# Kernel optimization log

Hardware: AMD Instinct MI355X
Metric: run time of the kernel (lower is better)

Reference implementation:

```python
import jax, jax.numpy as jnp
import numpy as np

KH, KW = 4, 4
N, P, IN_CH, OUT_CH = 50000, 32, 64, 64


def setup_inputs() -> dict:
    key = jax.random.key(0)
    k1, k2, k3, k4 = jax.random.split(key, 4)
    features = jax.random.normal(k1, (N, IN_CH), jnp.float32)
    receivers = jax.random.randint(k2, (N, P), 0, N)
    # relative offsets scaled so most neighbors fall inside the support radius
    relative_positions = jax.random.normal(k3, (N, P, 2), jnp.float32) * 0.35
    window_support = jnp.float32(1.0)
    a = 3  # window exponent (1 - d^2/R^2)^a
    kernel = jax.random.uniform(k4, (KH, KW, IN_CH, OUT_CH), jnp.float32, -0.05, 0.05)
    bias = jnp.zeros((OUT_CH,), jnp.float32)
    return {"features": features, "receivers": receivers,
            "relative_positions": relative_positions,
            "window_support": window_support, "a": a,
            "kernel": kernel, "bias": bias}


def reference(features, receivers, relative_positions, window_support, a, kernel, bias):
    kh, kw, in_ch, out_ch = kernel.shape
    n, p = receivers.shape
    g_bins = kh * kw

    gathered = features[receivers]                      # [N,P,in] gather
    r = relative_positions / window_support             # normalized to [-1,1]
    d2 = jnp.sum(r * r, axis=-1)                        # [N,P]
    win = jnp.maximum(1.0 - d2, 0.0) ** a               # radial window

    # map normalized position to continuous kernel-grid coordinates
    gy = jnp.clip((r[..., 0] + 1.0) * 0.5 * (kh - 1), 0.0, kh - 1)
    gx = jnp.clip((r[..., 1] + 1.0) * 0.5 * (kw - 1), 0.0, kw - 1)
    y0 = jnp.clip(jnp.floor(gy).astype(jnp.int32), 0, kh - 2)
    x0 = jnp.clip(jnp.floor(gx).astype(jnp.int32), 0, kw - 2)
    fy = gy - y0
    fx = gx - x0

    # accumulate window*bilinear-weighted features into kernel bins per output point,
    # avoiding materializing a per-edge [in,out] interpolated filter
    n_idx = jnp.arange(n)[:, None]                      # broadcasts over P
    M = jnp.zeros((n, g_bins, in_ch), features.dtype)
    corners = [(0, 0, (1 - fy) * (1 - fx)), (0, 1, (1 - fy) * fx),
               (1, 0, fy * (1 - fx)), (1, 1, fy * fx)]
    for dy, dx, bw in corners:
        g = (y0 + dy) * kw + (x0 + dx)                  # [N,P] flat bin index
        M = M.at[n_idx, g].add((bw * win)[..., None] * gathered)

    out = jnp.einsum('ngi,gio->no', M, kernel.reshape(g_bins, in_ch, out_ch))
    return out / p + bias
```

## Files before the change

kernel.cpp:

```cpp
#include <hip/hip_runtime.h>
#include <hip/hip_bf16.h>

typedef unsigned short u16;
typedef unsigned int u32;

#define THREADS 512
constexpr int CH = 64;
constexpr int PP = 32;
constexpr int TM = 16;

constexpr int W_OFF  = 0;
constexpr int RB_OFF = 0;
constexpr int MB_OFF = 16384;
constexpr int LDS_BYTES = 49152;

typedef __attribute__((ext_vector_type(8))) short short8;
typedef __attribute__((ext_vector_type(4))) float f32x4;

static __device__ __forceinline__ u16 f2bf_rne(float f) {
  __hip_bfloat16 h = __float2bfloat16(f);
  return __builtin_bit_cast(u16, h);
}
static __device__ __forceinline__ u16 rbf(float f) {
  u32 u = __builtin_bit_cast(u32, f);
  return (u16)((u + 0x8000u) >> 16);
}

__global__ void prep_all(const float* __restrict__ feat, u16* __restrict__ fbf,
                         const float* __restrict__ kern, u16* __restrict__ k2f,
                         int nq) {
  int i = blockIdx.x * blockDim.x + threadIdx.x;
  if (i < nq) {
    const int row = i >> 4, l15 = i & 15;
    const float* src = feat + (size_t)row * 64 + l15;
    const u32 a0 = f2bf_rne(src[0]);
    const u32 a1 = f2bf_rne(src[16]);
    const u32 a2 = f2bf_rne(src[32]);
    const u32 a3 = f2bf_rne(src[48]);
    uint2 w; w.x = a0 | (a1 << 16); w.y = a2 | (a3 << 16);
    ((uint2*)fbf)[i] = w;
  } else {
    const int d = i - nq;
    if (d < 65536) {
      const int e = d & 7, l = (d >> 3) & 63, ot = (d >> 9) & 3, ks = d >> 11;
      const int k = ks * 32 + (l >> 4) * 8 + e;
      const int o = ot * 16 + (l & 15);
      k2f[d] = f2bf_rne(kern[k * 64 + o]);
    }
  }
}

__global__ __launch_bounds__(THREADS, 6) void cconv_main(
    const int* __restrict__ recv, const float* __restrict__ relpos,
    const float* __restrict__ wsup, const int* __restrict__ aptr,
    const u16* __restrict__ fbf, const u16* __restrict__ k2f,
    const float* __restrict__ bias, float* __restrict__ out) {
  __shared__ __align__(16) char smem[LDS_BYTES];
  const int tid = threadIdx.x;
  const int n0 = blockIdx.x * TM;
  const int wid = tid >> 6, lane = tid & 63;
  const int l15 = lane & 15, l4 = lane >> 4;
  const int pairp = wid & 3;
  const int half  = wid >> 2;
  const char* fb2 = (const char*)fbf;

  const int* rp0 = recv + (n0 + wid * 2) * PP + l4 * 8;
  const int4 A40 = *(const int4*)rp0;
  const int4 B40 = *(const int4*)(rp0 + 4);
  const int4 A41 = *(const int4*)(rp0 + PP);
  const int4 B41 = *(const int4*)(rp0 + PP + 4);
  const int rv0[8] = {A40.x, A40.y, A40.z, A40.w, B40.x, B40.y, B40.z, B40.w};
  const int rv1[8] = {A41.x, A41.y, A41.z, A41.w, B41.x, B41.y, B41.z, B41.w};
  uint2 q20[8], q21[8];
  #pragma unroll
  for (int e = 0; e < 8; ++e)
    q20[e] = *(const uint2*)(fb2 + (size_t)(u32)rv0[e] * 128u + (u32)l15 * 8u);
  #pragma unroll
  for (int e = 0; e < 8; ++e)
    q21[e] = *(const uint2*)(fb2 + (size_t)(u32)rv1[e] * 128u + (u32)l15 * 8u);

  {
    const float invws = 1.0f / wsup[0];
    int a = aptr[0];
    if (a < 0 || a > 64) a = (int)(*(const float*)aptr);
    const int e = tid;
    const int m = e >> 5, p = e & 31;
    const int ei = (n0 + m) * PP + p;
    const float2 rp2 = ((const float2*)relpos)[ei];
    const float rx = rp2.x * invws, ry = rp2.y * invws;
    const float d2 = rx * rx + ry * ry;
    const float w1 = fmaxf(1.0f - d2, 0.0f);
    float win = 1.0f;
    for (int q = 0; q < a; ++q) win *= w1;
    float gy = fminf(fmaxf((rx + 1.0f) * 1.5f, 0.0f), 3.0f);
    float gx = fminf(fmaxf((ry + 1.0f) * 1.5f, 0.0f), 3.0f);
    int y0 = (int)gy; y0 = y0 > 2 ? 2 : y0;
    int x0 = (int)gx; x0 = x0 > 2 ? 2 : x0;
    const float fy = gy - (float)y0, fx = gx - (float)x0;
    u16* wp = (u16*)(smem + W_OFF) + m * 512 + p;
    #pragma unroll
    for (int g = 0; g < 16; ++g) {
      const int y = g >> 2, x = g & 3;
      const float wyv = (y == y0) ? (1.0f - fy) : (y == y0 + 1) ? fy : 0.0f;
      const float wxv = (x == x0) ? (1.0f - fx) : (x == x0 + 1) ? fx : 0.0f;
      wp[g * 32] = rbf(win * wyv * wxv);
    }
  }

  #pragma unroll
  for (int t = 0; t < 2; ++t) {
    const int m = wid * 2 + t;
    const short8 af = *(const short8*)(smem + W_OFF + m * 1024 + l15 * 64 + l4 * 16);
    const uint2* q2 = (t == 0) ? q20 : q21;
    f32x4 accm[4];
    const f32x4 cz = {0.f, 0.f, 0.f, 0.f};
    union { u32 u[4]; short8 s; } bb;
    #pragma unroll
    for (int j = 0; j < 4; ++j)
      bb.u[j] = (q2[2 * j].x & 0xffffu) | (q2[2 * j + 1].x << 16);
    accm[0] = __builtin_amdgcn_mfma_f32_16x16x32_bf16(af, bb.s, cz, 0, 0, 0);
    #pragma unroll
    for (int j = 0; j < 4; ++j)
      bb.u[j] = (q2[2 * j].x >> 16) | (q2[2 * j + 1].x & 0xffff0000u);
    accm[1] = __builtin_amdgcn_mfma_f32_16x16x32_bf16(af, bb.s, cz, 0, 0, 0);
    #pragma unroll
    for (int j = 0; j < 4; ++j)
      bb.u[j] = (q2[2 * j].y & 0xffffu) | (q2[2 * j + 1].y << 16);
    accm[2] = __builtin_amdgcn_mfma_f32_16x16x32_bf16(af, bb.s, cz, 0, 0, 0);
    #pragma unroll
    for (int j = 0; j < 4; ++j)
      bb.u[j] = (q2[2 * j].y >> 16) | (q2[2 * j + 1].y & 0xffff0000u);
    accm[3] = __builtin_amdgcn_mfma_f32_16x16x32_bf16(af, bb.s, cz, 0, 0, 0);
    #pragma unroll
    for (int ib = 0; ib < 4; ++ib)
      #pragma unroll
      for (int r = 0; r < 4; ++r) {
        const int g = l4 * 4 + r;
        const u32 k = (u32)(g * 64 + ib * 16 + l15);
        u32 byt = (u32)m * 2048u + k * 2u;
        byt ^= ((u32)((m & 7) ^ (g & 7)) << 4);
        *(u16*)(smem + MB_OFF + byt) = rbf(accm[ib][r]);
      }
  }
  __syncthreads();

  f32x4 acc = {0.f, 0.f, 0.f, 0.f};
  {
    const u32 rowb = (u32)l15 * 2048u;
    const u32 swl = (u32)(l15 & 7) << 4;
    #pragma unroll 8
    for (int j = 0; j < 16; ++j) {
      const int ks = half * 16 + j;
      const u32 kc = (u32)ks * 32u + (u32)l4 * 8u;
      const u32 g7 = (((kc >> 6) & 7u) << 4);
      const u32 byt = (rowb + kc * 2u) ^ swl ^ g7;
      const short8 a2 = *(const short8*)(smem + MB_OFF + byt);
      const short8 b2 = *(const short8*)(k2f + ((u32)(ks * 4 + pairp) * 64u + (u32)lane) * 8u);
      acc = __builtin_amdgcn_mfma_f32_16x16x32_bf16(a2, b2, acc, 0, 0, 0);
    }
  }

  if (half == 1) {
    #pragma unroll
    for (int r = 0; r < 4; ++r) {
      const int row = l4 * 4 + r;
      const u32 byt = (u32)pairp * 1024u + (u32)row * 64u + (u32)((l15 ^ l4) * 4);
      *(float*)(smem + RB_OFF + byt) = acc[r];
    }
  }
  __syncthreads();
  if (half == 0) {
    #pragma unroll
    for (int r = 0; r < 4; ++r) {
      const int row = l4 * 4 + r;
      const u32 byt = (u32)pairp * 1024u + (u32)row * 64u + (u32)((l15 ^ l4) * 4);
      acc[r] += *(const float*)(smem + RB_OFF + byt);
    }
    const int o = pairp * 16 + l15;
    const float bv = bias[o];
    #pragma unroll
    for (int r = 0; r < 4; ++r)
      out[(n0 + l4 * 4 + r) * CH + o] = acc[r] * (1.0f / 32.0f) + bv;
  }
}

extern "C" void kernel_launch(void* const* d_in, const int* in_sizes, int n_in,
                              void* d_out, int out_size, void* d_ws, size_t ws_size,
                              hipStream_t stream) {
  const float* features = (const float*)d_in[0];
  const int* receivers  = (const int*)d_in[1];
  const float* relpos   = (const float*)d_in[2];
  const float* wsup     = (const float*)d_in[3];
  const int* aptr       = (const int*)d_in[4];
  const float* kern     = (const float*)d_in[5];
  const float* bias     = (const float*)d_in[6];
  float* out = (float*)d_out;

  const int N = in_sizes[0] / CH;
  u16* fbf = (u16*)d_ws;
  u16* k2f = (u16*)((char*)d_ws + (size_t)N * CH * 2);

  const int nq = N * 16;
  const int prep_total = nq + 65536;
  prep_all<<<dim3((prep_total + 255) / 256), dim3(256), 0, stream>>>(
      features, fbf, kern, k2f, nq);

  cconv_main<<<dim3(N / TM), dim3(THREADS), 0, stream>>>(
      receivers, relpos, wsup, aptr, fbf, k2f, bias, out);
}
```

Measured before the change: 48.76 us.

## Make main kernel persistent and keep filter weights resident in registers

The main kernel now runs on a fixed grid of 625 blocks. Each block loops over several 16-point tiles instead of handling a single one. The bf16 filter fragments, bias, window scale and exponent are loaded once per block, with the filter kept in 16 short8 registers, instead of being re-read from global memory for every tile. The reduction buffer moves to its own LDS region so it does not clash with the next tile's window writes, and the launch bound drops from 6 to 4 blocks per CU. The goal is less repeated filter traffic and less per-block setup, at the cost of higher register pressure, fewer resident waves to hide the gather latency, and no overlap between tiles within a block.

```diff
diff --git a/kernel.cpp b/kernel.cpp
--- a/kernel.cpp
+++ b/kernel.cpp
@@ -8,11 +8,12 @@
 constexpr int CH = 64;
 constexpr int PP = 32;
 constexpr int TM = 16;
+constexpr int GRID = 625;
 
 constexpr int W_OFF  = 0;
-constexpr int RB_OFF = 0;
 constexpr int MB_OFF = 16384;
-constexpr int LDS_BYTES = 49152;
+constexpr int RB_OFF = 49152;
+constexpr int LDS_BYTES = 53248;
 
 typedef __attribute__((ext_vector_type(8))) short short8;
 typedef __attribute__((ext_vector_type(4))) float f32x4;
@@ -50,137 +51,147 @@
   }
 }
 
-__global__ __launch_bounds__(THREADS, 6) void cconv_main(
+__global__ __launch_bounds__(THREADS, 4) void cconv_main(
     const int* __restrict__ recv, const float* __restrict__ relpos,
     const float* __restrict__ wsup, const int* __restrict__ aptr,
     const u16* __restrict__ fbf, const u16* __restrict__ k2f,
-    const float* __restrict__ bias, float* __restrict__ out) {
+    const float* __restrict__ bias, float* __restrict__ out, int ntile) {
   __shared__ __align__(16) char smem[LDS_BYTES];
   const int tid = threadIdx.x;
-  const int n0 = blockIdx.x * TM;
   const int wid = tid >> 6, lane = tid & 63;
   const int l15 = lane & 15, l4 = lane >> 4;
   const int pairp = wid & 3;
   const int half  = wid >> 2;
   const char* fb2 = (const char*)fbf;
 
-  const int* rp0 = recv + (n0 + wid * 2) * PP + l4 * 8;
-  const int4 A40 = *(const int4*)rp0;
-  const int4 B40 = *(const int4*)(rp0 + 4);
-  const int4 A41 = *(const int4*)(rp0 + PP);
-  const int4 B41 = *(const int4*)(rp0 + PP + 4);
-  const int rv0[8] = {A40.x, A40.y, A40.z, A40.w, B40.x, B40.y, B40.z, B40.w};
-  const int rv1[8] = {A41.x, A41.y, A41.z, A41.w, B41.x, B41.y, B41.z, B41.w};
-  uint2 q20[8], q21[8];
+  short8 b2r[16];
   #pragma unroll
-  for (int e = 0; e < 8; ++e)
-    q20[e] = *(const uint2*)(fb2 + (size_t)(u32)rv0[e] * 128u + (u32)l15 * 8u);
-  #pragma unroll
-  for (int e = 0; e < 8; ++e)
-    q21[e] = *(const uint2*)(fb2 + (size_t)(u32)rv1[e] * 128u + (u32)l15 * 8u);
-
-  {
-    const float invws = 1.0f / wsup[0];
-    int a = aptr[0];
-    if (a < 0 || a > 64) a = (int)(*(const float*)aptr);
-    const int e = tid;
-    const int m = e >> 5, p = e & 31;
-    const int ei = (n0 + m) * PP + p;
-    const float2 rp2 = ((const float2*)relpos)[ei];
-    const float rx = rp2.x * invws, ry = rp2.y * invws;
-    const float d2 = rx * rx + ry * ry;
-    const float w1 = fmaxf(1.0f - d2, 0.0f);
-    float win = 1.0f;
-    for (int q = 0; q < a; ++q) win *= w1;
-    float gy = fminf(fmaxf((rx + 1.0f) * 1.5f, 0.0f), 3.0f);
-    float gx = fminf(fmaxf((ry + 1.0f) * 1.5f, 0.0f), 3.0f);
-    int y0 = (int)gy; y0 = y0 > 2 ? 2 : y0;
-    int x0 = (int)gx; x0 = x0 > 2 ? 2 : x0;
-    const float fy = gy - (float)y0, fx = gx - (float)x0;
-    u16* wp = (u16*)(smem + W_OFF) + m * 512 + p;
+  for (int j = 0; j < 16; ++j)
+    b2r[j] = *(const short8*)(k2f +
+        ((u32)((half * 16 + j) * 4 + pairp) * 64u + (u32)lane) * 8u);
+
+  const float invws = 1.0f / wsup[0];
+  int aexp = aptr[0];
+  if (aexp < 0 || aexp > 64) aexp = (int)(*(const float*)aptr);
+  const float bv = bias[pairp * 16 + l15];
+
+  for (int tile = blockIdx.x; tile < ntile; tile += GRID) {
+    const int n0 = tile * TM;
+
+    const int* rp0 = recv + (n0 + wid * 2) * PP + l4 * 8;
+    const int4 A40 = *(const int4*)rp0;
+    const int4 B40 = *(const int4*)(rp0 + 4);
+    const int4 A41 = *(const int4*)(rp0 + PP);
+    const int4 B41 = *(const int4*)(rp0 + PP + 4);
+    const int rv0[8] = {A40.x, A40.y, A40.z, A40.w, B40.x, B40.y, B40.z, B40.w};
+    const int rv1[8] = {A41.x, A41.y, A41.z, A41.w, B41.x, B41.y, B41.z, B41.w};
+    uint2 q20[8], q21[8];
     #pragma unroll
-    for (int g = 0; g < 16; ++g) {
-      const int y = g >> 2, x = g & 3;
-      const float wyv = (y == y0) ? (1.0f - fy) : (y == y0 + 1) ? fy : 0.0f;
-      const float wxv = (x == x0) ? (1.0f - fx) : (x == x0 + 1) ? fx : 0.0f;
-      wp[g * 32] = rbf(win * wyv * wxv);
-    }
-  }
-
-  #pragma unroll
-  for (int t = 0; t < 2; ++t) {
-    const int m = wid * 2 + t;
-    const short8 af = *(const short8*)(smem + W_OFF + m * 1024 + l15 * 64 + l4 * 16);
-    const uint2* q2 = (t == 0) ? q20 : q21;
-    f32x4 accm[4];
-    const f32x4 cz = {0.f, 0.f, 0.f, 0.f};
-    union { u32 u[4]; short8 s; } bb;
+    for (int e = 0; e < 8; ++e)
+      q20[e] = *(const uint2*)(fb2 + (size_t)(u32)rv0[e] * 128u + (u32)l15 * 8u);
     #pragma unroll
-    for (int j = 0; j < 4; ++j)
-      bb.u[j] = (q2[2 * j].x & 0xffffu) | (q2[2 * j + 1].x << 16);
-    accm[0] = __builtin_amdgcn_mfma_f32_16x16x32_bf16(af, bb.s, cz, 0, 0, 0);
+    for (int e = 0; e < 8; ++e)
+      q21[e] = *(const uint2*)(fb2 + (size_t)(u32)rv1[e] * 128u + (u32)l15 * 8u);
+
+    {
+      const int e = tid;
+      const int m = e >> 5, p = e & 31;
+      const int ei = (n0 + m) * PP + p;
+      const float2 rp2 = ((const float2*)relpos)[ei];
+      const float rx = rp2.x * invws, ry = rp2.y * invws;
+      const float d2 = rx * rx + ry * ry;
+      const float w1 = fmaxf(1.0f - d2, 0.0f);
+      float win = 1.0f;
+      for (int q = 0; q < aexp; ++q) win *= w1;
+      float gy = fminf(fmaxf((rx + 1.0f) * 1.5f, 0.0f), 3.0f);
+      float gx = fminf(fmaxf((ry + 1.0f) * 1.5f, 0.0f), 3.0f);
+      int y0 = (int)gy; y0 = y0 > 2 ? 2 : y0;
+      int x0 = (int)gx; x0 = x0 > 2 ? 2 : x0;
+      const float fy = gy - (float)y0, fx = gx - (float)x0;
+      u16* wp = (u16*)(smem + W_OFF) + m * 512 + p;
+      #pragma unroll
+      for (int g = 0; g < 16; ++g) {
+        const int y = g >> 2, x = g & 3;
+        const float wyv = (y == y0) ? (1.0f - fy) : (y == y0 + 1) ? fy : 0.0f;
+        const float wxv = (x == x0) ? (1.0f - fx) : (x == x0 + 1) ? fx : 0.0f;
+        wp[g * 32] = rbf(win * wyv * wxv);
+      }
+    }
+
     #pragma unroll
-    for (int j = 0; j < 4; ++j)
-      bb.u[j] = (q2[2 * j].x >> 16) | (q2[2 * j + 1].x & 0xffff0000u);
-    accm[1] = __builtin_amdgcn_mfma_f32_16x16x32_bf16(af, bb.s, cz, 0, 0, 0);
-    #pragma unroll
-    for (int j = 0; j < 4; ++j)
-      bb.u[j] = (q2[2 * j].y & 0xffffu) | (q2[2 * j + 1].y << 16);
-    accm[2] = __builtin_amdgcn_mfma_f32_16x16x32_bf16(af, bb.s, cz, 0, 0, 0);
-    #pragma unroll
-    for (int j = 0; j < 4; ++j)
-      bb.u[j] = (q2[2 * j].y >> 16) | (q2[2 * j + 1].y & 0xffff0000u);
-    accm[3] = __builtin_amdgcn_mfma_f32_16x16x32_bf16(af, bb.s, cz, 0, 0, 0);
-    #pragma unroll
-    for (int ib = 0; ib < 4; ++ib)
+    for (int t = 0; t < 2; ++t) {
+      const int m = wid * 2 + t;
+      const short8 af = *(const short8*)(smem + W_OFF + m * 1024 + l15 * 64 + l4 * 16);
+      const uint2* q2 = (t == 0) ? q20 : q21;
+      f32x4 accm[4];
+      const f32x4 cz = {0.f, 0.f, 0.f, 0.f};
+      union { u32 u[4]; short8 s; } bb;
+      #pragma unroll
+      for (int j = 0; j < 4; ++j)
+        bb.u[j] = (q2[2 * j].x & 0xffffu) | (q2[2 * j + 1].x << 16);
+      accm[0] = __builtin_amdgcn_mfma_f32_16x16x32_bf16(af, bb.s, cz, 0, 0, 0);
+      #pragma unroll
+      for (int j = 0; j < 4; ++j)
+        bb.u[j] = (q2[2 * j].x >> 16) | (q2[2 * j + 1].x & 0xffff0000u);
+      accm[1] = __builtin_amdgcn_mfma_f32_16x16x32_bf16(af, bb.s, cz, 0, 0, 0);
+      #pragma unroll
+      for (int j = 0; j < 4; ++j)
+        bb.u[j] = (q2[2 * j].y & 0xffffu) | (q2[2 * j + 1].y << 16);
+      accm[2] = __builtin_amdgcn_mfma_f32_16x16x32_bf16(af, bb.s, cz, 0, 0, 0);
+      #pragma unroll
+      for (int j = 0; j < 4; ++j)
+        bb.u[j] = (q2[2 * j].y >> 16) | (q2[2 * j + 1].y & 0xffff0000u);
+      accm[3] = __builtin_amdgcn_mfma_f32_16x16x32_bf16(af, bb.s, cz, 0, 0, 0);
+      #pragma unroll
+      for (int ib = 0; ib < 4; ++ib)
+        #pragma unroll
+        for (int r = 0; r < 4; ++r) {
+          const int g = l4 * 4 + r;
+          const u32 k = (u32)(g * 64 + ib * 16 + l15);
+          u32 byt = (u32)m * 2048u + k * 2u;
+          byt ^= ((u32)((m & 7) ^ (g & 7)) << 4);
+          *(u16*)(smem + MB_OFF + byt) = rbf(accm[ib][r]);
+        }
+    }
+    __syncthreads();
+
+    f32x4 acc = {0.f, 0.f, 0.f, 0.f};
+    {
+      const u32 rowb = (u32)l15 * 2048u;
+      const u32 swl = (u32)(l15 & 7) << 4;
+      #pragma unroll
+      for (int j = 0; j < 16; ++j) {
+        const int ks = half * 16 + j;
+        const u32 kc = (u32)ks * 32u + (u32)l4 * 8u;
+        const u32 g7 = (((kc >> 6) & 7u) << 4);
+        const u32 byt = (rowb + kc * 2u) ^ swl ^ g7;
+        const short8 a2 = *(const short8*)(smem + MB_OFF + byt);
+        acc = __builtin_amdgcn_mfma_f32_16x16x32_bf16(a2, b2r[j], acc, 0, 0, 0);
+        if ((j & 1) == 1) __builtin_amdgcn_sched_barrier(0);
+      }
+    }
+
+    if (half == 1) {
       #pragma unroll
       for (int r = 0; r < 4; ++r) {
-        const int g = l4 * 4 + r;
-        const u32 k = (u32)(g * 64 + ib * 16 + l15);
-        u32 byt = (u32)m * 2048u + k * 2u;
-        byt ^= ((u32)((m & 7) ^ (g & 7)) << 4);
-        *(u16*)(smem + MB_OFF + byt) = rbf(accm[ib][r]);
-      }
-  }
-  __syncthreads();
-
-  f32x4 acc = {0.f, 0.f, 0.f, 0.f};
-  {
-    const u32 rowb = (u32)l15 * 2048u;
-    const u32 swl = (u32)(l15 & 7) << 4;
-    #pragma unroll 8
-    for (int j = 0; j < 16; ++j) {
-      const int ks = half * 16 + j;
-      const u32 kc = (u32)ks * 32u + (u32)l4 * 8u;
-      const u32 g7 = (((kc >> 6) & 7u) << 4);
-      const u32 byt = (rowb + kc * 2u) ^ swl ^ g7;
-      const short8 a2 = *(const short8*)(smem + MB_OFF + byt);
-      const short8 b2 = *(const short8*)(k2f + ((u32)(ks * 4 + pairp) * 64u + (u32)lane) * 8u);
-      acc = __builtin_amdgcn_mfma_f32_16x16x32_bf16(a2, b2, acc, 0, 0, 0);
-    }
-  }
-
-  if (half == 1) {
-    #pragma unroll
-    for (int r = 0; r < 4; ++r) {
-      const int row = l4 * 4 + r;
-      const u32 byt = (u32)pairp * 1024u + (u32)row * 64u + (u32)((l15 ^ l4) * 4);
-      *(float*)(smem + RB_OFF + byt) = acc[r];
-    }
-  }
-  __syncthreads();
-  if (half == 0) {
-    #pragma unroll
-    for (int r = 0; r < 4; ++r) {
-      const int row = l4 * 4 + r;
-      const u32 byt = (u32)pairp * 1024u + (u32)row * 64u + (u32)((l15 ^ l4) * 4);
-      acc[r] += *(const float*)(smem + RB_OFF + byt);
-    }
-    const int o = pairp * 16 + l15;
-    const float bv = bias[o];
-    #pragma unroll
-    for (int r = 0; r < 4; ++r)
-      out[(n0 + l4 * 4 + r) * CH + o] = acc[r] * (1.0f / 32.0f) + bv;
+        const int row = l4 * 4 + r;
+        const u32 byt = (u32)pairp * 1024u + (u32)row * 64u + (u32)((l15 ^ l4) * 4);
+        *(float*)(smem + RB_OFF + byt) = acc[r];
+      }
+    }
+    __syncthreads();
+    if (half == 0) {
+      #pragma unroll
+      for (int r = 0; r < 4; ++r) {
+        const int row = l4 * 4 + r;
+        const u32 byt = (u32)pairp * 1024u + (u32)row * 64u + (u32)((l15 ^ l4) * 4);
+        acc[r] += *(const float*)(smem + RB_OFF + byt);
+      }
+      const int o = pairp * 16 + l15;
+      #pragma unroll
+      for (int r = 0; r < 4; ++r)
+        out[(n0 + l4 * 4 + r) * CH + o] = acc[r] * (1.0f / 32.0f) + bv;
+    }
   }
 }
 
@@ -205,6 +216,7 @@
   prep_all<<<dim3((prep_total + 255) / 256), dim3(256), 0, stream>>>(
       features, fbf, kern, k2f, nq);
 
-  cconv_main<<<dim3(N / TM), dim3(THREADS), 0, stream>>>(
-      receivers, relpos, wsup, aptr, fbf, k2f, bias, out);
-}
+  const int ntile = N / TM;
+  cconv_main<<<dim3(GRID), dim3(THREADS), 0, stream>>>(
+      receivers, relpos, wsup, aptr, fbf, k2f, bias, out, ntile);
+}
```

New measurement: 146.7 us. 201% more time.
